# Optimization experiments

Measured on AMD Instinct MI355X. Metric: run time of the kernel, lower is better.

Reference implementation:

```python
import jax, jax.numpy as jnp
import numpy as np

N = 50000   # nodes
E = 800000  # edges
F = 64      # num_node_features
H = 64      # hidden_channels
NB = 3      # num_blocks
G = 64      # graphs in batch
C = 10      # num_classes
EPS = 1e-5  # BatchNorm eps


def setup_inputs() -> dict:
    key = jax.random.key(0)
    ks = jax.random.split(key, 24)
    x = jax.random.normal(ks[0], (N, F), dtype=jnp.float32)
    edge_index = jax.random.randint(ks[1], (2, E), 0, N, dtype=jnp.int64)
    batch = jnp.sort(jax.random.randint(ks[2], (N,), 0, G, dtype=jnp.int64))
    s = 0.05
    inp = {
        "x": x, "edge_index": edge_index, "batch": batch,
        "pre_w": jax.random.normal(ks[3], (F, H)) * s,
        "pre_b": jnp.zeros((H,), jnp.float32),
        # stacked per-block params (blocks are structurally identical)
        "blk_prelu1": jnp.full((NB,), 0.25, jnp.float32),
        "blk_bn_gamma": jnp.ones((NB, H), jnp.float32),
        "blk_bn_beta": jnp.zeros((NB, H), jnp.float32),
        "blk_w1": jax.random.normal(ks[4], (NB, H, 2 * H)) * s,
        "blk_b1": jnp.zeros((NB, 2 * H), jnp.float32),
        "blk_prelu2": jnp.full((NB,), 0.25, jnp.float32),
        "blk_w2": jax.random.normal(ks[5], (NB, 2 * H, H)) * s,
        "blk_b2": jnp.zeros((NB, H), jnp.float32),
        "post_bn_gamma": jnp.ones((H,), jnp.float32),
        "post_bn_beta": jnp.zeros((H,), jnp.float32),
        "fc1_w": jax.random.normal(ks[6], (H, 4 * H)) * s,
        "fc1_b": jnp.zeros((4 * H,), jnp.float32),
        "post_prelu": jnp.asarray(0.25, jnp.float32),
        "fc2_w": jax.random.normal(ks[7], (4 * H, C)) * s,
        "fc2_b": jnp.zeros((C,), jnp.float32),
    }
    return inp


def _prelu(x, a):
    return jnp.where(x >= 0, x, a * x)


def _batchnorm(x, gamma, beta):
    # training-mode BN over the node dimension (biased variance), as in torch
    mean = jnp.mean(x, axis=0)
    var = jnp.var(x, axis=0)
    return (x - mean) * jax.lax.rsqrt(var + EPS) * gamma + beta


def _gcn_conv(x, W, bias, src, dst):
    # PyG GCNConv: linear transform, then D^-1/2 (A+I) D^-1/2 aggregation, then bias.
    h = x @ W                                   # [N, out]
    deg = jax.ops.segment_sum(jnp.ones((E,), h.dtype), dst, num_segments=N) + 1.0
    dinv = jax.lax.rsqrt(deg)                   # [N]
    norm = dinv[src] * dinv[dst]                # [E]
    agg = jax.ops.segment_sum(h[src] * norm[:, None], dst, num_segments=N)
    agg = agg + h * (dinv * dinv)[:, None]      # self-loop contribution
    return agg + bias


def reference(x, edge_index, batch, pre_w, pre_b,
              blk_prelu1, blk_bn_gamma, blk_bn_beta, blk_w1, blk_b1,
              blk_prelu2, blk_w2, blk_b2,
              post_bn_gamma, post_bn_beta, fc1_w, fc1_b, post_prelu, fc2_w, fc2_b):
    src, dst = edge_index[0], edge_index[1]
    h = x @ pre_w + pre_b                       # [N, H]
    for i in range(NB):
        h = _prelu(h, blk_prelu1[i])
        h = _batchnorm(h, blk_bn_gamma[i], blk_bn_beta[i])
        h = _gcn_conv(h, blk_w1[i], blk_b1[i], src, dst)   # [N, 2H]
        h = _prelu(h, blk_prelu2[i])
        h = _gcn_conv(h, blk_w2[i], blk_b2[i], src, dst)   # [N, H]
    # global mean pool per graph
    sums = jax.ops.segment_sum(h, batch, num_segments=G)   # [G, H]
    cnts = jax.ops.segment_sum(jnp.ones((N,), h.dtype), batch, num_segments=G)
    pooled = sums / jnp.maximum(cnts, 1.0)[:, None]
    out = _batchnorm(pooled, post_bn_gamma, post_bn_beta)
    out = out @ fc1_w + fc1_b
    out = _prelu(out, post_prelu)
    # dropout with p=0.0 is identity
    out = out @ fc2_w + fc2_b                   # [G, C]
    return out
```

## Files before the change

### kernel.cpp

```cpp
#include <hip/hip_runtime.h>
#include <hip/hip_fp16.h>

#define NN 50000
#define NE 800000
#define NG 64
#define NC 10
#define BN_EPS 1e-5f
#define NSB 196

typedef __attribute__((ext_vector_type(2))) _Float16 h2v;
typedef __attribute__((ext_vector_type(8))) _Float16 f16x8;
typedef __attribute__((ext_vector_type(4))) float f32x4;

__device__ __forceinline__ float2 up2(unsigned u) {
    __half2 h = *reinterpret_cast<__half2*>(&u);
    return __half22float2(h);
}
__device__ __forceinline__ unsigned pk2(float a, float b) {
    __half2 h = __floats2half2_rn(a, b);
    return *reinterpret_cast<unsigned*>(&h);
}
__device__ __forceinline__ float fdot2u(unsigned a, unsigned b, float c) {
    return __builtin_amdgcn_fdot2(__builtin_bit_cast(h2v, a), __builtin_bit_cast(h2v, b), c, false);
}


__global__ void deg_count_kernel(const int* __restrict__ dst, int* __restrict__ deg,
                                 unsigned short* __restrict__ pos16) {
    int e = blockIdx.x * blockDim.x + threadIdx.x;
    if (e < NE) {
        int d = __builtin_nontemporal_load(&dst[e]);
        unsigned short p = (unsigned short)atomicAdd(&deg[d], 1);
        __builtin_nontemporal_store(p, &pos16[e]);
    }
}

__global__ __launch_bounds__(256) void block_sum_kernel(const int* __restrict__ deg,
                                                        int* __restrict__ bsum) {
    int b = blockIdx.x, t = threadIdx.x;
    int n = b * 256 + t;
    int v = (n < NN) ? deg[n] : 0;
    __shared__ int red[256];
    red[t] = v;
    __syncthreads();
    for (int off = 128; off > 0; off >>= 1) {
        if (t < off) red[t] += red[t + off];
        __syncthreads();
    }
    if (t == 0) bsum[b] = red[0];
}

__global__ __launch_bounds__(256) void bsum_scan_kernel(const int* __restrict__ bsum,
                                                        int* __restrict__ boff) {
    __shared__ int s[256];
    int t = threadIdx.x;
    int v = (t < NSB) ? bsum[t] : 0;
    s[t] = v;
    __syncthreads();
    for (int off = 1; off < 256; off <<= 1) {
        int cur = s[t];
        int add = (t >= off) ? s[t - off] : 0;
        __syncthreads();
        s[t] = cur + add;
        __syncthreads();
    }
    if (t < NSB) boff[t] = s[t] - v;
}

__global__ __launch_bounds__(256) void csr_setup_kernel(const int* __restrict__ deg,
                                                        const int* __restrict__ boff,
                                                        int* __restrict__ row_off,
                                                        float* __restrict__ dinv,
                                                        float* __restrict__ rdeg) {
    int b = blockIdx.x, t = threadIdx.x;
    int n = b * 256 + t;
    int v = (n < NN) ? deg[n] : 0;
    __shared__ int s[256];
    s[t] = v;
    __syncthreads();
    for (int off = 1; off < 256; off <<= 1) {
        int cur = s[t];
        int add = (t >= off) ? s[t - off] : 0;
        __syncthreads();
        s[t] = cur + add;
        __syncthreads();
    }
    int excl = s[t] - v + boff[b];
    if (n < NN) {
        row_off[n] = excl;
        float d = (float)v + 1.0f;
        dinv[n] = rsqrtf(d);
        rdeg[n] = sqrtf(d);
    }
    if (n == NN - 1) row_off[NN] = NE;
}

__global__ void scatter_csr_kernel(const int* __restrict__ src, const int* __restrict__ dst,
                                   const unsigned short* __restrict__ pos16,
                                   const int* __restrict__ row_off,
                                   int* __restrict__ csr_src) {
    int e = blockIdx.x * blockDim.x + threadIdx.x;
    if (e >= NE) return;
    int s = __builtin_nontemporal_load(&src[e]);
    int d = __builtin_nontemporal_load(&dst[e]);
    int p = (int)__builtin_nontemporal_load(&pos16[e]);
    csr_src[row_off[d] + p] = s;
}

__global__ void arow_kernel(const int* __restrict__ row_off, const int* __restrict__ csr_src,
                            const float* __restrict__ dinv, float* __restrict__ arow) {
    int n = blockIdx.x * 256 + threadIdx.x;
    if (n >= NN) return;
    float dv = dinv[n];
    float s = dv;
    int e0 = row_off[n], e1 = row_off[n + 1];
    for (int i = e0; i < e1; ++i) s += dinv[csr_src[i]];
    arow[n] = dv * s;
}


__global__ __launch_bounds__(256) void bn_stats_kernel(const __half* __restrict__ h,
                                                       const float* __restrict__ rdeg,
                                                       const float* __restrict__ alpha_p,
                                                       float* __restrict__ stats) {
    float alpha = alpha_p[0];
    int tid = threadIdx.x;
    int c4 = (tid & 15) * 4;
    int rg = tid >> 4;
    float sx = 0, sy = 0, sz = 0, sw = 0;
    float qx = 0, qy = 0, qz = 0, qw = 0;
    for (int n = blockIdx.x * 16 + rg; n < NN; n += gridDim.x * 16) {
        float rd = rdeg[n];
        uint2 u = *(const uint2*)&h[(size_t)n * 64 + c4];
        float2 lo = up2(u.x), hi = up2(u.y);
        float a = lo.x >= 0.f ? lo.x : alpha * lo.x;
        float b = lo.y >= 0.f ? lo.y : alpha * lo.y;
        float c = hi.x >= 0.f ? hi.x : alpha * hi.x;
        float d = hi.y >= 0.f ? hi.y : alpha * hi.y;
        a *= rd; b *= rd; c *= rd; d *= rd;
        sx += a; sy += b; sz += c; sw += d;
        qx += a * a; qy += b * b; qz += c * c; qw += d * d;
    }
    __shared__ float ls[256 * 8];
    float* p = &ls[tid * 8];
    p[0] = sx; p[1] = sy; p[2] = sz; p[3] = sw;
    p[4] = qx; p[5] = qy; p[6] = qz; p[7] = qw;
    __syncthreads();
    if (tid < 128) {
        int cidx = tid >> 3;
        int j = tid & 7;
        float acc = 0.f;
        for (int r = 0; r < 16; ++r) acc += ls[(r * 16 + cidx) * 8 + j];
        int ch = cidx * 4 + (j & 3);
        if (j < 4) atomicAdd(&stats[ch], acc);
        else       atomicAdd(&stats[64 + ch], acc);
    }
}


template <bool PRELU, int OUT>
__global__ __launch_bounds__(256) void gather_kernel(const int* __restrict__ row_off,
                                                     const int* __restrict__ csr_src,
                                                     const float* __restrict__ dinv,
                                                     const float* __restrict__ bias,
                                                     const float* __restrict__ alpha_p,
                                                     const __half* __restrict__ hh,
                                                     __half* __restrict__ outp) {
    int tid = threadIdx.x;
    int r = blockIdx.x * 32 + (tid >> 3);
    int c = blockIdx.y * 32 + (tid & 7) * 4;
    if (r >= NN) return;
    float alpha = 0.f;
    if constexpr (PRELU) alpha = alpha_p[0];
    uint2 u0 = *(const uint2*)&hh[(size_t)r * 64 + c];
    float2 slo = up2(u0.x), shi = up2(u0.y);
    float ax = slo.x, ay = slo.y, az = shi.x, aw = shi.y;
    if constexpr (PRELU) {
        ax = ax >= 0.f ? ax : alpha * ax;
        ay = ay >= 0.f ? ay : alpha * ay;
        az = az >= 0.f ? az : alpha * az;
        aw = aw >= 0.f ? aw : alpha * aw;
    }
    int beg = row_off[r];
    int end = row_off[r + 1];
    int nct = (end - beg + 7) >> 3;
    int base = beg;
    int q[8];
    if (nct > 0) {
#pragma unroll
        for (int j = 0; j < 8; ++j) {
            int pos = base + j;
            q[j] = csr_src[pos < end ? pos : end - 1];
        }
    }
    for (int it = 0; it < nct; ++it) {
        int s[8];
#pragma unroll
        for (int j = 0; j < 8; ++j) s[j] = q[j];
        int cbase = base;
        base += 8;
        if (it + 1 < nct) {
#pragma unroll
            for (int j = 0; j < 8; ++j) {
                int pos = base + j;
                q[j] = csr_src[pos < end ? pos : end - 1];
            }
        }
        uint2 v[8];
#pragma unroll
        for (int j = 0; j < 8; ++j) v[j] = *(const uint2*)&hh[(size_t)s[j] * 64 + c];
#pragma unroll
        for (int j = 0; j < 8; ++j) {
            float m = (cbase + j < end) ? 1.f : 0.f;
            float2 a = up2(v[j].x), b = up2(v[j].y);
            if constexpr (PRELU) {
                a.x = a.x >= 0.f ? a.x : alpha * a.x;
                a.y = a.y >= 0.f ? a.y : alpha * a.y;
                b.x = b.x >= 0.f ? b.x : alpha * b.x;
                b.y = b.y >= 0.f ? b.y : alpha * b.y;
            }
            ax = fmaf(a.x, m, ax);
            ay = fmaf(a.y, m, ay);
            az = fmaf(b.x, m, az);
            aw = fmaf(b.y, m, aw);
        }
    }
    float dv = dinv[r];
    float ox, oy, oz, ow;
    if constexpr (OUT == 2) {
        ox = dv * ax; oy = dv * ay; oz = dv * az; ow = dv * aw;
    } else {
        float4 b = *(const float4*)&bias[c];
        ox = dv * ax + b.x; oy = dv * ay + b.y; oz = dv * az + b.z; ow = dv * aw + b.w;
        if constexpr (OUT == 1) {
            ox *= dv; oy *= dv; oz *= dv; ow *= dv;
        }
    }
    uint2 o;
    o.x = pk2(ox, oy);
    o.y = pk2(oz, ow);
    *(uint2*)&outp[(size_t)r * 64 + c] = o;
}


__global__ __launch_bounds__(256) void gemm_pre_kernel(const float* __restrict__ Af,
                                                       const float* __restrict__ W,
                                                       __half* __restrict__ outp,
                                                       const float* __restrict__ bias,
                                                       const float* __restrict__ dinv) {
    constexpr int K = 64, M = 64, BM = 128;
    constexpr int CG = M / 8;
    constexpr int RG = 256 / CG;
    constexpr int KP = K / 2;
    __shared__ unsigned Wh[KP * M];
    __shared__ unsigned Ahs[BM][KP + 4];
    int tid = threadIdx.x;
    for (int i = tid; i < KP * M; i += 256) {
        int kp = i / M, j = i % M;
        Wh[i] = pk2(W[(2 * kp) * M + j], W[(2 * kp + 1) * M + j]);
    }
    int r0 = blockIdx.x * BM;
    for (int i = tid; i < BM * (K / 4); i += 256) {
        int row = i / (K / 4);
        int k4 = (i % (K / 4)) * 4;
        int rr = r0 + row;
        if (rr > NN - 1) rr = NN - 1;
        float4 v = *(const float4*)&Af[(size_t)rr * K + k4];
        uint2 o;
        o.x = pk2(v.x, v.y);
        o.y = pk2(v.z, v.w);
        *(uint2*)&Ahs[row][k4 >> 1] = o;
    }
    __syncthreads();
    int cg = tid % CG, rg = tid / CG;
    int c = cg * 8;
    float acc[4][8];
#pragma unroll
    for (int r = 0; r < 4; ++r)
#pragma unroll
        for (int j = 0; j < 8; ++j) acc[r][j] = 0.f;
#pragma unroll 4
    for (int kp = 0; kp < KP; kp += 2) {
        uint2 a2[4];
#pragma unroll
        for (int r = 0; r < 4; ++r) a2[r] = *(const uint2*)&Ahs[rg + r * RG][kp];
#pragma unroll
        for (int kk = 0; kk < 2; ++kk) {
            const unsigned* wp = &Wh[(kp + kk) * M + c];
            uint4 w0 = *(const uint4*)wp;
            uint4 w1 = *(const uint4*)(wp + 4);
#pragma unroll
            for (int r = 0; r < 4; ++r) {
                unsigned av = kk ? a2[r].y : a2[r].x;
                acc[r][0] = fdot2u(av, w0.x, acc[r][0]);
                acc[r][1] = fdot2u(av, w0.y, acc[r][1]);
                acc[r][2] = fdot2u(av, w0.z, acc[r][2]);
                acc[r][3] = fdot2u(av, w0.w, acc[r][3]);
                acc[r][4] = fdot2u(av, w1.x, acc[r][4]);
                acc[r][5] = fdot2u(av, w1.y, acc[r][5]);
                acc[r][6] = fdot2u(av, w1.z, acc[r][6]);
                acc[r][7] = fdot2u(av, w1.w, acc[r][7]);
            }
        }
    }
    float4 b0 = *(const float4*)&bias[c];
    float4 b1 = *(const float4*)&bias[c + 4];
#pragma unroll
    for (int r = 0; r < 4; ++r) {
        int row = r0 + rg + r * RG;
        if (row < NN) {
            float sc = dinv[row];
            uint4 o;
            o.x = pk2((acc[r][0] + b0.x) * sc, (acc[r][1] + b0.y) * sc);
            o.y = pk2((acc[r][2] + b0.z) * sc, (acc[r][3] + b0.w) * sc);
            o.z = pk2((acc[r][4] + b1.x) * sc, (acc[r][5] + b1.y) * sc);
            o.w = pk2((acc[r][6] + b1.z) * sc, (acc[r][7] + b1.w) * sc);
            *(uint4*)&outp[(size_t)row * M + c] = o;
        }
    }
}


__global__ __launch_bounds__(256) void mfma_gemm1_kernel(const __half* __restrict__ t,
                                                         const float* __restrict__ W1,
                                                         const float* __restrict__ b1,
                                                         __half* __restrict__ u,
                                                         const float* __restrict__ stats,
                                                         const float* __restrict__ gamma,
                                                         const float* __restrict__ beta,
                                                         const float* __restrict__ arow) {
    __shared__ _Float16 At[128][72];
    __shared__ _Float16 Wt[128][72];
    __shared__ float scS[64], shS[64];
    int tid = threadIdx.x;
    if (tid < 64) {
        float mean = stats[tid] * (1.0f / NN);
        float var  = stats[64 + tid] * (1.0f / NN) - mean * mean;
        float sc = gamma[tid] * rsqrtf(var + BN_EPS);
        scS[tid] = sc;
        shS[tid] = beta[tid] - mean * sc;
    }
    for (int i = tid; i < 128 * 32; i += 256) {
        int j = i & 127;
        int k2 = i >> 7;
        *(unsigned*)&Wt[j][2 * k2] = pk2(W1[(2 * k2) * 128 + j], W1[(2 * k2 + 1) * 128 + j]);
    }
    __syncthreads();
    int r0 = blockIdx.x * 128;
    for (int i = tid; i < 128 * 16; i += 256) {
        int row = i >> 4;
        int k4 = (i & 15) * 4;
        int rr = r0 + row;
        if (rr > NN - 1) rr = NN - 1;
        uint2 uu = *(const uint2*)&t[(size_t)rr * 64 + k4];
        float2 lo = up2(uu.x), hi = up2(uu.y);
        float av = arow[rr];
        float vx = lo.x * scS[k4 + 0] + shS[k4 + 0] * av;
        float vy = lo.y * scS[k4 + 1] + shS[k4 + 1] * av;
        float vz = hi.x * scS[k4 + 2] + shS[k4 + 2] * av;
        float vw = hi.y * scS[k4 + 3] + shS[k4 + 3] * av;
        *(unsigned*)&At[row][k4]     = pk2(vx, vy);
        *(unsigned*)&At[row][k4 + 2] = pk2(vz, vw);
    }
    __syncthreads();
    int w = tid >> 6;
    int l = tid & 63;
    int lr = l & 15;
    int lk = (l >> 4) * 8;
    f32x4 acc[2][8];
#pragma unroll
    for (int rt = 0; rt < 2; ++rt)
#pragma unroll
        for (int ct = 0; ct < 8; ++ct) acc[rt][ct] = (f32x4){0.f, 0.f, 0.f, 0.f};
#pragma unroll
    for (int k0 = 0; k0 < 64; k0 += 32) {
        f16x8 a0 = *(const f16x8*)&At[w * 32 + lr][k0 + lk];
        f16x8 a1 = *(const f16x8*)&At[w * 32 + 16 + lr][k0 + lk];
#pragma unroll
        for (int ct = 0; ct < 8; ++ct) {
            f16x8 b = *(const f16x8*)&Wt[ct * 16 + lr][k0 + lk];
            acc[0][ct] = __builtin_amdgcn_mfma_f32_16x16x32_f16(a0, b, acc[0][ct], 0, 0, 0);
            acc[1][ct] = __builtin_amdgcn_mfma_f32_16x16x32_f16(a1, b, acc[1][ct], 0, 0, 0);
        }
    }
    int rowbase = r0 + w * 32 + (l >> 4) * 4;
#pragma unroll
    for (int rt = 0; rt < 2; ++rt) {
#pragma unroll
        for (int ct = 0; ct < 8; ++ct) {
            int col = ct * 16 + lr;
            float bb = b1[col];
#pragma unroll
            for (int r = 0; r < 4; ++r) {
                int row = rowbase + rt * 16 + r;
                if (row < NN) u[(size_t)row * 128 + col] = __float2half(acc[rt][ct][r] + bb);
            }
        }
    }
}


__global__ __launch_bounds__(256) void mfma_gemm2_kernel(const __half* __restrict__ u,
                                                         const float* __restrict__ W2,
                                                         const float* __restrict__ alpha_p,
                                                         const float* __restrict__ dinv,
                                                         __half* __restrict__ t) {
    __shared__ _Float16 Ut[64][136];
    __shared__ _Float16 Wt[64][136];
    int tid = threadIdx.x;
    float alpha = alpha_p[0];
    for (int i = tid; i < 64 * 64; i += 256) {
        int j = i & 63;
        int k2 = i >> 6;
        *(unsigned*)&Wt[j][2 * k2] = pk2(W2[(2 * k2) * 64 + j], W2[(2 * k2 + 1) * 64 + j]);
    }
    int r0 = blockIdx.x * 64;
    for (int i = tid; i < 64 * 32; i += 256) {
        int row = i >> 5;
        int k4 = (i & 31) * 4;
        int rr = r0 + row;
        if (rr > NN - 1) rr = NN - 1;
        uint2 uu = *(const uint2*)&u[(size_t)rr * 128 + k4];
        float2 lo = up2(uu.x), hi = up2(uu.y);
        float vx = lo.x >= 0.f ? lo.x : alpha * lo.x;
        float vy = lo.y >= 0.f ? lo.y : alpha * lo.y;
        float vz = hi.x >= 0.f ? hi.x : alpha * hi.x;
        float vw = hi.y >= 0.f ? hi.y : alpha * hi.y;
        *(unsigned*)&Ut[row][k4]     = pk2(vx, vy);
        *(unsigned*)&Ut[row][k4 + 2] = pk2(vz, vw);
    }
    __syncthreads();
    int w = tid >> 6;
    int l = tid & 63;
    int lr = l & 15;
    int lk = (l >> 4) * 8;
    f32x4 acc[4];
#pragma unroll
    for (int ct = 0; ct < 4; ++ct) acc[ct] = (f32x4){0.f, 0.f, 0.f, 0.f};
#pragma unroll
    for (int k0 = 0; k0 < 128; k0 += 32) {
        f16x8 a = *(const f16x8*)&Ut[w * 16 + lr][k0 + lk];
#pragma unroll
        for (int ct = 0; ct < 4; ++ct) {
            f16x8 b = *(const f16x8*)&Wt[ct * 16 + lr][k0 + lk];
            acc[ct] = __builtin_amdgcn_mfma_f32_16x16x32_f16(a, b, acc[ct], 0, 0, 0);
        }
    }
    int rowbase = r0 + w * 16 + (l >> 4) * 4;
#pragma unroll
    for (int ct = 0; ct < 4; ++ct) {
        int col = ct * 16 + lr;
#pragma unroll
        for (int r = 0; r < 4; ++r) {
            int row = rowbase + r;
            if (row < NN) t[(size_t)row * 64 + col] = __float2half(acc[ct][r] * dinv[row]);
        }
    }
}


__global__ __launch_bounds__(256) void pool_seg_kernel(const __half* __restrict__ h,
                                                       const int* __restrict__ batch,
                                                       float* __restrict__ pooled) {
    int g = blockIdx.x;
    __shared__ int sbeg, send;
    int tid = threadIdx.x;
    if (tid == 0) {
        int lo = 0, hi = NN;
        while (lo < hi) { int mid = (lo + hi) >> 1; if (batch[mid] < g) lo = mid + 1; else hi = mid; }
        sbeg = lo;
        lo = 0; hi = NN;
        while (lo < hi) { int mid = (lo + hi) >> 1; if (batch[mid] < g + 1) lo = mid + 1; else hi = mid; }
        send = lo;
    }
    __syncthreads();
    int beg = sbeg, end = send;
    int c4 = (tid & 15) * 4;
    int rg = tid >> 4;
    float sx = 0, sy = 0, sz = 0, sw = 0;
    for (int n = beg + rg; n < end; n += 16) {
        uint2 u = *(const uint2*)&h[(size_t)n * 64 + c4];
        float2 lo = up2(u.x), hi = up2(u.y);
        sx += lo.x; sy += lo.y; sz += hi.x; sw += hi.y;
    }
    __shared__ float red[256 * 4];
    float* p = &red[tid * 4];
    p[0] = sx; p[1] = sy; p[2] = sz; p[3] = sw;
    __syncthreads();
    if (tid < 64) {
        int cg = tid >> 2;
        int j = tid & 3;
        float acc = 0.f;
        for (int r = 0; r < 16; ++r) acc += red[(r * 16 + cg) * 4 + j];
        float cnt = fmaxf((float)(end - beg), 1.0f);
        pooled[g * 64 + cg * 4 + j] = acc / cnt;
    }
}


__global__ __launch_bounds__(64) void head_stats_kernel(const float* __restrict__ pooled,
                                                        const float* __restrict__ gamma,
                                                        const float* __restrict__ beta,
                                                        float* __restrict__ headsc) {
    int ch = threadIdx.x;
    float s = 0.f, q = 0.f;
    for (int g = 0; g < 64; ++g) {
        float v = pooled[g * 64 + ch];
        s += v; q += v * v;
    }
    float mean = s * (1.0f / 64.0f);
    float var = q * (1.0f / 64.0f) - mean * mean;
    float sc = gamma[ch] * rsqrtf(var + BN_EPS);
    headsc[ch] = sc;
    headsc[64 + ch] = beta[ch] - mean * sc;
}

__global__ __launch_bounds__(256) void head_fc_kernel(const float* __restrict__ pooled,
                                                      const float* __restrict__ headsc,
                                                      const float* __restrict__ fc1w,
                                                      const float* __restrict__ fc1b,
                                                      const float* __restrict__ prelu_p,
                                                      const float* __restrict__ fc2w,
                                                      const float* __restrict__ fc2b,
                                                      float* __restrict__ out) {
    int g = blockIdx.x;
    int tid = threadIdx.x;
    __shared__ float pr[64];
    __shared__ float red[256];
    if (tid < 64) pr[tid] = pooled[g * 64 + tid] * headsc[tid] + headsc[64 + tid];
    __syncthreads();
    float alpha = prelu_p[0];
    float o1 = fc1b[tid];
    for (int k = 0; k < 64; ++k) o1 += pr[k] * fc1w[k * 256 + tid];
    o1 = o1 >= 0.f ? o1 : alpha * o1;
    for (int c = 0; c < NC; ++c) {
        red[tid] = o1 * fc2w[tid * NC + c];
        __syncthreads();
        for (int off = 128; off > 0; off >>= 1) {
            if (tid < off) red[tid] += red[tid + off];
            __syncthreads();
        }
        if (tid == 0) out[g * NC + c] = red[0] + fc2b[c];
        __syncthreads();
    }
}


extern "C" void kernel_launch(void* const* d_in, const int* in_sizes, int n_in,
                              void* d_out, int out_size, void* d_ws, size_t ws_size,
                              hipStream_t stream) {
    const float* x       = (const float*)d_in[0];
    const int*   ei      = (const int*)d_in[1];
    const int*   batch   = (const int*)d_in[2];
    const float* pre_w   = (const float*)d_in[3];
    const float* pre_b   = (const float*)d_in[4];
    const float* bp1     = (const float*)d_in[5];
    const float* bng     = (const float*)d_in[6];
    const float* bnb     = (const float*)d_in[7];
    const float* bw1     = (const float*)d_in[8];
    const float* bb1     = (const float*)d_in[9];
    const float* bp2     = (const float*)d_in[10];
    const float* bw2     = (const float*)d_in[11];
    const float* bb2     = (const float*)d_in[12];
    const float* pgamma  = (const float*)d_in[13];
    const float* pbeta   = (const float*)d_in[14];
    const float* fc1w    = (const float*)d_in[15];
    const float* fc1b    = (const float*)d_in[16];
    const float* pprelu  = (const float*)d_in[17];
    const float* fc2w    = (const float*)d_in[18];
    const float* fc2b    = (const float*)d_in[19];

    const int* src = ei;
    const int* dst = ei + NE;

    __half* hA16 = (__half*)d_ws;
    __half* t16  = hA16 + (size_t)NN * 64;
    __half* u16  = t16 + (size_t)NN * 64;
    float* dinv  = (float*)(u16 + (size_t)NN * 128);
    float* rdeg  = dinv + NN;
    float* arow  = rdeg + NN;
    float* stats = arow + NN;
    float* pooledg = stats + 3 * 128;
    float* headsc  = pooledg + 64 * 64;
    int*   csr_src = (int*)(headsc + 128);
    int*   row_off = csr_src + NE;
    int*   deg     = row_off + NN + 1;
    int*   bsum    = deg + NN;
    int*   boff    = bsum + NSB;
    unsigned short* pos16 = (unsigned short*)(boff + NSB);

    hipMemsetAsync(stats, 0, (size_t)3 * 128 * 4, stream);
    hipMemsetAsync(deg, 0, (size_t)NN * 4, stream);

    deg_count_kernel<<<(NE + 255) / 256, 256, 0, stream>>>(dst, deg, pos16);
    block_sum_kernel<<<NSB, 256, 0, stream>>>(deg, bsum);
    bsum_scan_kernel<<<1, 256, 0, stream>>>(bsum, boff);
    csr_setup_kernel<<<NSB, 256, 0, stream>>>(deg, boff, row_off, dinv, rdeg);
    scatter_csr_kernel<<<(NE + 255) / 256, 256, 0, stream>>>(src, dst, pos16, row_off, csr_src);
    arow_kernel<<<(NN + 255) / 256, 256, 0, stream>>>(row_off, csr_src, dinv, arow);

    gemm_pre_kernel<<<(NN + 127) / 128, 256, 0, stream>>>(x, pre_w, hA16, pre_b, dinv);

    dim3 ggrid((NN + 31) / 32, 2);
    for (int i = 0; i < 3; ++i) {
        const float* a1 = bp1 + i;
        const float* a2 = bp2 + i;
        const float* gm = bng + i * 64;
        const float* bt = bnb + i * 64;
        const float* w1 = bw1 + (size_t)i * 64 * 128;
        const float* b1 = bb1 + i * 128;
        const float* w2 = bw2 + (size_t)i * 128 * 64;
        const float* b2 = bb2 + i * 64;
        float* st = stats + i * 128;

        bn_stats_kernel<<<256, 256, 0, stream>>>(hA16, rdeg, a1, st);
        gather_kernel<true, 2><<<ggrid, 256, 0, stream>>>(
            row_off, csr_src, dinv, nullptr, a1, hA16, t16);
        mfma_gemm1_kernel<<<(NN + 127) / 128, 256, 0, stream>>>(
            t16, w1, b1, u16, st, gm, bt, arow);
        mfma_gemm2_kernel<<<(NN + 63) / 64, 256, 0, stream>>>(
            u16, w2, a2, dinv, t16);
        if (i < 2) {
            gather_kernel<false, 1><<<ggrid, 256, 0, stream>>>(
                row_off, csr_src, dinv, b2, nullptr, t16, hA16);
        } else {
            gather_kernel<false, 0><<<ggrid, 256, 0, stream>>>(
                row_off, csr_src, dinv, b2, nullptr, t16, hA16);
        }
    }

    pool_seg_kernel<<<NG, 256, 0, stream>>>(hA16, batch, pooledg);
    head_stats_kernel<<<1, 64, 0, stream>>>(pooledg, pgamma, pbeta, headsc);
    head_fc_kernel<<<NG, 256, 0, stream>>>(pooledg, headsc, fc1w, fc1b, pprelu,
                                           fc2w, fc2b, (float*)d_out);
}
```

Baseline: 385.1 us.

## Fuse the two per-block GEMMs into one MLP kernel and split CSR scatter into passes

Merges the first and second GCN linear transforms into a single kernel that keeps the 128-wide intermediate in shared memory, applying bias and PReLU on the fly. This removes the global round trip of the intermediate tensor and one launch per block. The CSR scatter is also split into four passes by destination range to localize scattered writes, at the cost of re-reading the destination array each pass. The two memsets are merged by moving the degree buffer next to the stats buffer.

Measured after the change: 368.8 us. 1.04x faster.

```diff
diff --git a/kernel.cpp b/kernel.cpp
--- a/kernel.cpp
+++ b/kernel.cpp
@@ -95,14 +95,15 @@
     if (n == NN - 1) row_off[NN] = NE;
 }
 
-__global__ void scatter_csr_kernel(const int* __restrict__ src, const int* __restrict__ dst,
-                                   const unsigned short* __restrict__ pos16,
-                                   const int* __restrict__ row_off,
-                                   int* __restrict__ csr_src) {
+__global__ void scatter_pass_kernel(const int* __restrict__ src, const int* __restrict__ dst,
+                                    const unsigned short* __restrict__ pos16,
+                                    const int* __restrict__ row_off,
+                                    int* __restrict__ csr_src, int d0, int d1) {
     int e = blockIdx.x * blockDim.x + threadIdx.x;
     if (e >= NE) return;
+    int d = __builtin_nontemporal_load(&dst[e]);
+    if (d < d0 || d >= d1) return;
     int s = __builtin_nontemporal_load(&src[e]);
-    int d = __builtin_nontemporal_load(&dst[e]);
     int p = (int)__builtin_nontemporal_load(&pos16[e]);
     csr_src[row_off[d] + p] = s;
 }
@@ -321,16 +322,21 @@
 }
 
 
-__global__ __launch_bounds__(256) void mfma_gemm1_kernel(const __half* __restrict__ t,
-                                                         const float* __restrict__ W1,
-                                                         const float* __restrict__ b1,
-                                                         __half* __restrict__ u,
-                                                         const float* __restrict__ stats,
-                                                         const float* __restrict__ gamma,
-                                                         const float* __restrict__ beta,
-                                                         const float* __restrict__ arow) {
-    __shared__ _Float16 At[128][72];
-    __shared__ _Float16 Wt[128][72];
+__global__ __launch_bounds__(256) void mfma_mlp_kernel(__half* __restrict__ t,
+                                                       const float* __restrict__ W1,
+                                                       const float* __restrict__ b1,
+                                                       const float* __restrict__ W2,
+                                                       const float* __restrict__ alpha2_p,
+                                                       const float* __restrict__ stats,
+                                                       const float* __restrict__ gamma,
+                                                       const float* __restrict__ beta,
+                                                       const float* __restrict__ arow,
+                                                       const float* __restrict__ dinv) {
+    __shared__ __align__(16) char smem[45056];
+    auto Wt1 = (_Float16(*)[72])smem;
+    auto Wt2 = (_Float16(*)[136])smem;
+    auto At  = (_Float16(*)[72])(smem + 18432);
+    auto Ut  = (_Float16(*)[136])(smem + 27648);
     __shared__ float scS[64], shS[64];
     int tid = threadIdx.x;
     if (tid < 64) {
@@ -343,11 +349,10 @@
     for (int i = tid; i < 128 * 32; i += 256) {
         int j = i & 127;
         int k2 = i >> 7;
-        *(unsigned*)&Wt[j][2 * k2] = pk2(W1[(2 * k2) * 128 + j], W1[(2 * k2 + 1) * 128 + j]);
-    }
-    __syncthreads();
-    int r0 = blockIdx.x * 128;
-    for (int i = tid; i < 128 * 16; i += 256) {
+        *(unsigned*)&Wt1[j][2 * k2] = pk2(W1[(2 * k2) * 128 + j], W1[(2 * k2 + 1) * 128 + j]);
+    }
+    int r0 = blockIdx.x * 64;
+    for (int i = tid; i < 64 * 16; i += 256) {
         int row = i >> 4;
         int k4 = (i & 15) * 4;
         int rr = r0 + row;
@@ -367,93 +372,61 @@
     int l = tid & 63;
     int lr = l & 15;
     int lk = (l >> 4) * 8;
-    f32x4 acc[2][8];
-#pragma unroll
-    for (int rt = 0; rt < 2; ++rt)
-#pragma unroll
-        for (int ct = 0; ct < 8; ++ct) acc[rt][ct] = (f32x4){0.f, 0.f, 0.f, 0.f};
-#pragma unroll
-    for (int k0 = 0; k0 < 64; k0 += 32) {
-        f16x8 a0 = *(const f16x8*)&At[w * 32 + lr][k0 + lk];
-        f16x8 a1 = *(const f16x8*)&At[w * 32 + 16 + lr][k0 + lk];
-#pragma unroll
-        for (int ct = 0; ct < 8; ++ct) {
-            f16x8 b = *(const f16x8*)&Wt[ct * 16 + lr][k0 + lk];
-            acc[0][ct] = __builtin_amdgcn_mfma_f32_16x16x32_f16(a0, b, acc[0][ct], 0, 0, 0);
-            acc[1][ct] = __builtin_amdgcn_mfma_f32_16x16x32_f16(a1, b, acc[1][ct], 0, 0, 0);
-        }
-    }
-    int rowbase = r0 + w * 32 + (l >> 4) * 4;
-#pragma unroll
-    for (int rt = 0; rt < 2; ++rt) {
+    int rloc = w * 16 + (l >> 4) * 4;
+    {
+        f32x4 acc[8];
+#pragma unroll
+        for (int ct = 0; ct < 8; ++ct) acc[ct] = (f32x4){0.f, 0.f, 0.f, 0.f};
+#pragma unroll
+        for (int k0 = 0; k0 < 64; k0 += 32) {
+            f16x8 a = *(const f16x8*)&At[w * 16 + lr][k0 + lk];
+#pragma unroll
+            for (int ct = 0; ct < 8; ++ct) {
+                f16x8 b = *(const f16x8*)&Wt1[ct * 16 + lr][k0 + lk];
+                acc[ct] = __builtin_amdgcn_mfma_f32_16x16x32_f16(a, b, acc[ct], 0, 0, 0);
+            }
+        }
+        float alpha = alpha2_p[0];
 #pragma unroll
         for (int ct = 0; ct < 8; ++ct) {
             int col = ct * 16 + lr;
             float bb = b1[col];
 #pragma unroll
             for (int r = 0; r < 4; ++r) {
-                int row = rowbase + rt * 16 + r;
-                if (row < NN) u[(size_t)row * 128 + col] = __float2half(acc[rt][ct][r] + bb);
+                float v = acc[ct][r] + bb;
+                v = v >= 0.f ? v : alpha * v;
+                Ut[rloc + r][col] = (_Float16)v;
             }
         }
     }
-}
-
-
-__global__ __launch_bounds__(256) void mfma_gemm2_kernel(const __half* __restrict__ u,
-                                                         const float* __restrict__ W2,
-                                                         const float* __restrict__ alpha_p,
-                                                         const float* __restrict__ dinv,
-                                                         __half* __restrict__ t) {
-    __shared__ _Float16 Ut[64][136];
-    __shared__ _Float16 Wt[64][136];
-    int tid = threadIdx.x;
-    float alpha = alpha_p[0];
+    __syncthreads();
     for (int i = tid; i < 64 * 64; i += 256) {
         int j = i & 63;
         int k2 = i >> 6;
-        *(unsigned*)&Wt[j][2 * k2] = pk2(W2[(2 * k2) * 64 + j], W2[(2 * k2 + 1) * 64 + j]);
-    }
-    int r0 = blockIdx.x * 64;
-    for (int i = tid; i < 64 * 32; i += 256) {
-        int row = i >> 5;
-        int k4 = (i & 31) * 4;
-        int rr = r0 + row;
-        if (rr > NN - 1) rr = NN - 1;
-        uint2 uu = *(const uint2*)&u[(size_t)rr * 128 + k4];
-        float2 lo = up2(uu.x), hi = up2(uu.y);
-        float vx = lo.x >= 0.f ? lo.x : alpha * lo.x;
-        float vy = lo.y >= 0.f ? lo.y : alpha * lo.y;
-        float vz = hi.x >= 0.f ? hi.x : alpha * hi.x;
-        float vw = hi.y >= 0.f ? hi.y : alpha * hi.y;
-        *(unsigned*)&Ut[row][k4]     = pk2(vx, vy);
-        *(unsigned*)&Ut[row][k4 + 2] = pk2(vz, vw);
-    }
-    __syncthreads();
-    int w = tid >> 6;
-    int l = tid & 63;
-    int lr = l & 15;
-    int lk = (l >> 4) * 8;
-    f32x4 acc[4];
-#pragma unroll
-    for (int ct = 0; ct < 4; ++ct) acc[ct] = (f32x4){0.f, 0.f, 0.f, 0.f};
-#pragma unroll
-    for (int k0 = 0; k0 < 128; k0 += 32) {
-        f16x8 a = *(const f16x8*)&Ut[w * 16 + lr][k0 + lk];
+        *(unsigned*)&Wt2[j][2 * k2] = pk2(W2[(2 * k2) * 64 + j], W2[(2 * k2 + 1) * 64 + j]);
+    }
+    __syncthreads();
+    {
+        f32x4 acc[4];
+#pragma unroll
+        for (int ct = 0; ct < 4; ++ct) acc[ct] = (f32x4){0.f, 0.f, 0.f, 0.f};
+#pragma unroll
+        for (int k0 = 0; k0 < 128; k0 += 32) {
+            f16x8 a = *(const f16x8*)&Ut[w * 16 + lr][k0 + lk];
+#pragma unroll
+            for (int ct = 0; ct < 4; ++ct) {
+                f16x8 b = *(const f16x8*)&Wt2[ct * 16 + lr][k0 + lk];
+                acc[ct] = __builtin_amdgcn_mfma_f32_16x16x32_f16(a, b, acc[ct], 0, 0, 0);
+            }
+        }
 #pragma unroll
         for (int ct = 0; ct < 4; ++ct) {
-            f16x8 b = *(const f16x8*)&Wt[ct * 16 + lr][k0 + lk];
-            acc[ct] = __builtin_amdgcn_mfma_f32_16x16x32_f16(a, b, acc[ct], 0, 0, 0);
-        }
-    }
-    int rowbase = r0 + w * 16 + (l >> 4) * 4;
-#pragma unroll
-    for (int ct = 0; ct < 4; ++ct) {
-        int col = ct * 16 + lr;
-#pragma unroll
-        for (int r = 0; r < 4; ++r) {
-            int row = rowbase + r;
-            if (row < NN) t[(size_t)row * 64 + col] = __float2half(acc[ct][r] * dinv[row]);
+            int col = ct * 16 + lr;
+#pragma unroll
+            for (int r = 0; r < 4; ++r) {
+                int row = r0 + rloc + r;
+                if (row < NN) t[(size_t)row * 64 + col] = __float2half(acc[ct][r] * dinv[row]);
+            }
         }
     }
 }
@@ -575,28 +548,31 @@
 
     __half* hA16 = (__half*)d_ws;
     __half* t16  = hA16 + (size_t)NN * 64;
-    __half* u16  = t16 + (size_t)NN * 64;
-    float* dinv  = (float*)(u16 + (size_t)NN * 128);
+    float* dinv  = (float*)(t16 + (size_t)NN * 64);
     float* rdeg  = dinv + NN;
     float* arow  = rdeg + NN;
     float* stats = arow + NN;
-    float* pooledg = stats + 3 * 128;
+    int*   deg   = (int*)(stats + 3 * 128);
+    float* pooledg = (float*)(deg + NN);
     float* headsc  = pooledg + 64 * 64;
     int*   csr_src = (int*)(headsc + 128);
     int*   row_off = csr_src + NE;
-    int*   deg     = row_off + NN + 1;
-    int*   bsum    = deg + NN;
+    int*   bsum    = row_off + NN + 1;
     int*   boff    = bsum + NSB;
     unsigned short* pos16 = (unsigned short*)(boff + NSB);
 
-    hipMemsetAsync(stats, 0, (size_t)3 * 128 * 4, stream);
-    hipMemsetAsync(deg, 0, (size_t)NN * 4, stream);
+    hipMemsetAsync(stats, 0, ((size_t)3 * 128 + NN) * 4, stream);
 
     deg_count_kernel<<<(NE + 255) / 256, 256, 0, stream>>>(dst, deg, pos16);
     block_sum_kernel<<<NSB, 256, 0, stream>>>(deg, bsum);
     bsum_scan_kernel<<<1, 256, 0, stream>>>(bsum, boff);
     csr_setup_kernel<<<NSB, 256, 0, stream>>>(deg, boff, row_off, dinv, rdeg);
-    scatter_csr_kernel<<<(NE + 255) / 256, 256, 0, stream>>>(src, dst, pos16, row_off, csr_src);
+    for (int p = 0; p < 4; ++p) {
+        int d0 = p * 12500;
+        int d1 = (p == 3) ? NN : d0 + 12500;
+        scatter_pass_kernel<<<(NE + 255) / 256, 256, 0, stream>>>(
+            src, dst, pos16, row_off, csr_src, d0, d1);
+    }
     arow_kernel<<<(NN + 255) / 256, 256, 0, stream>>>(row_off, csr_src, dinv, arow);
 
     gemm_pre_kernel<<<(NN + 127) / 128, 256, 0, stream>>>(x, pre_w, hA16, pre_b, dinv);
@@ -616,10 +592,8 @@
         bn_stats_kernel<<<256, 256, 0, stream>>>(hA16, rdeg, a1, st);
         gather_kernel<true, 2><<<ggrid, 256, 0, stream>>>(
             row_off, csr_src, dinv, nullptr, a1, hA16, t16);
-        mfma_gemm1_kernel<<<(NN + 127) / 128, 256, 0, stream>>>(
-            t16, w1, b1, u16, st, gm, bt, arow);
-        mfma_gemm2_kernel<<<(NN + 63) / 64, 256, 0, stream>>>(
-            u16, w2, a2, dinv, t16);
+        mfma_mlp_kernel<<<(NN + 63) / 64, 256, 0, stream>>>(
+            t16, w1, b1, w2, a2, st, gm, bt, arow, dinv);
         if (i < 2) {
             gather_kernel<false, 1><<<ggrid, 256, 0, stream>>>(
                 row_off, csr_src, dinv, b2, nullptr, t16, hA16);
```
